# Optimization experiments

Measured on AMD Instinct MI355X. Metric: run time of the kernel, lower is better.

The kernel has to match this reference:

```python
import jax, jax.numpy as jnp
import numpy as np

B, IN, OUT = 128, 1024, 1024
BETA, THRESHOLD, RESET = 0.99, 1.0, 0.8
TAU_POS, TAU_NEG = 20.0, 20.0
A_POS, A_NEG = 0.005, 0.005


def setup_inputs() -> dict:
    key = jax.random.key(0)
    k1, k2, k3, k4, k5 = jax.random.split(key, 5)
    in_spikes = (jax.random.uniform(k1, (B, IN)) < 0.1).astype(jnp.float32)
    # nn.Linear default init: U(-1/sqrt(in), 1/sqrt(in))
    bound = 1.0 / np.sqrt(IN)
    W = jax.random.uniform(k2, (OUT, IN), minval=-bound, maxval=bound, dtype=jnp.float32)
    membrane = jax.random.normal(k3, (B, OUT), dtype=jnp.float32) * 0.5
    # trace timers (time since last spike), random in [0, 50)
    delta_pre = jax.random.uniform(k4, (B, IN), dtype=jnp.float32) * 50.0
    delta_fire = jax.random.uniform(k5, (B, OUT), dtype=jnp.float32) * 50.0
    return {"in_spikes": in_spikes, "W": W, "membrane": membrane,
            "delta_pre": delta_pre, "delta_fire": delta_fire}


def reference(in_spikes, W, membrane, delta_pre, delta_fire):
    # dense projection (bias is unused in the original forward)
    weighted = jnp.matmul(in_spikes, W.T)                      # (B, OUT)
    # LIF neuron
    mem = membrane * BETA + weighted
    spike = (mem > THRESHOLD).astype(jnp.float32)
    mem = jnp.where(spike > 0, mem - RESET, mem)
    # trace updates: increment, reset-to-zero where a spike occurred
    dp = jnp.where(in_spikes > 0, 0.0, delta_pre + 1.0)        # (B, IN)
    df = jnp.where(spike > 0, 0.0, delta_fire + 1.0)           # (B, OUT)
    # pairwise timing difference: (B, IN, OUT)
    delta_t = df[:, None, :] - dp[:, :, None]
    potentiation = (delta_t > 0) * (A_POS * jnp.exp(-delta_t / TAU_POS))
    depression = (delta_t < 0) * (A_NEG * jnp.exp(delta_t / TAU_NEG))
    weight_changes = potentiation - depression                 # (B, IN, OUT)
    avg_weight_changes = weight_changes.mean(axis=0).T         # (OUT, IN)
    new_W = W + avg_weight_changes
    return spike, new_W, mem
```

## Files before the change

kernel.cpp:

```cpp
#include <hip/hip_runtime.h>
#include <cstdint>
#include <cmath>

#define Bb   128
#define INN  1024
#define OUTN 1024
#define A_TOT   (0.005f / 128.0f)
#define INV_TAU (1.0f / 20.0f)

__device__ __forceinline__ uint32_t rne_bf16(float f) {
    uint32_t u = __float_as_uint(f);
    return (u + 0x7fffu + ((u >> 16) & 1u)) >> 16;
}

__global__ __launch_bounds__(256) void prep_k(
    const float* __restrict__ W, const float* __restrict__ in_spikes,
    const float* __restrict__ delta_pre,
    float* __restrict__ Wt, uint32_t* __restrict__ IPackT,
    int* __restrict__ gIdx, int* __restrict__ gCount) {
    __shared__ float tile[32][33];
    const int blk = blockIdx.x;
    const int t   = threadIdx.x;

    if ((blk & 3) == 0 && t < 64) {
        const int b = blk >> 2;
        int base = 0;
#pragma unroll
        for (int c = 0; c < 16; c++) {
            float s = in_spikes[(size_t)b * INN + c * 64 + t];
            unsigned long long m = __ballot(s > 0.0f);
            if (s > 0.0f) {
                int pos = base + __popcll(m & ((1ULL << t) - 1ULL));
                gIdx[b * INN + pos] = c * 64 + t;
            }
            base += __popcll(m);
        }
        if (t == 0) gCount[b] = base;
    }

    {
        const int e = blk * 256 + t;
        const int b = e >> 10, i = e & 1023;
        float sp = in_spikes[e];
        float dp = (sp > 0.0f) ? 0.0f : delta_pre[e] + 1.0f;
        float Iz = expf(-dp * INV_TAU);
        float Iy = A_TOT * expf(dp * INV_TAU);
        IPackT[(size_t)i * Bb + b] = (rne_bf16(Iz) << 16) | rne_bf16(Iy);
    }

    const int x = t & 31, y = t >> 5;
#pragma unroll
    for (int k = 0; k < 2; k++) {
        int tau = blk * 2 + k;
        int bx = tau & 31, by = tau >> 5;
        __syncthreads();
#pragma unroll
        for (int j = 0; j < 4; j++)
            tile[y + j * 8][x] = W[(size_t)(by * 32 + y + j * 8) * INN + bx * 32 + x];
        __syncthreads();
#pragma unroll
        for (int j = 0; j < 4; j++)
            Wt[(size_t)(bx * 32 + y + j * 8) * OUTN + by * 32 + x] = tile[x][y + j * 8];
    }
}

__global__ __launch_bounds__(256) void spmv_lif_k(
    const float* __restrict__ Wt, const float* __restrict__ membrane,
    const float* __restrict__ delta_fire,
    const int* __restrict__ gIdx, const int* __restrict__ gCount,
    uint32_t* __restrict__ OPackT,
    float* __restrict__ out_spike, float* __restrict__ out_mem) {
    __shared__ int sIdx[INN];
    const int b = blockIdx.x;
    const int z = blockIdx.y;
    const int t = threadIdx.x;
    const int n = gCount[b];
    for (int j = t; j < n; j += 256) sIdx[j] = gIdx[b * INN + j];
    __syncthreads();

    const int o = z * 256 + t;
    float acc = 0.0f;
    int j = 0;
    for (; j + 8 <= n; j += 8) {
        float w0 = Wt[(size_t)sIdx[j + 0] * OUTN + o];
        float w1 = Wt[(size_t)sIdx[j + 1] * OUTN + o];
        float w2 = Wt[(size_t)sIdx[j + 2] * OUTN + o];
        float w3 = Wt[(size_t)sIdx[j + 3] * OUTN + o];
        float w4 = Wt[(size_t)sIdx[j + 4] * OUTN + o];
        float w5 = Wt[(size_t)sIdx[j + 5] * OUTN + o];
        float w6 = Wt[(size_t)sIdx[j + 6] * OUTN + o];
        float w7 = Wt[(size_t)sIdx[j + 7] * OUTN + o];
        acc += ((w0 + w1) + (w2 + w3)) + ((w4 + w5) + (w6 + w7));
    }
    for (; j < n; j++) acc += Wt[(size_t)sIdx[j] * OUTN + o];

    const int n_bo = b * OUTN + o;
    float mem = membrane[n_bo] * 0.99f + acc;
    float s = (mem > 1.0f) ? 1.0f : 0.0f;
    mem = (s > 0.0f) ? mem - 0.8f : mem;
    out_spike[n_bo] = s;
    out_mem[n_bo] = mem;

    float df = (s > 0.0f) ? 0.0f : delta_fire[n_bo] + 1.0f;
    float Oy = expf(-df * INV_TAU);
    float Oz = -A_TOT * expf(df * INV_TAU);
    OPackT[(size_t)o * Bb + b] = (rne_bf16(Oy) << 16) | rne_bf16(Oz);
}

__global__ __launch_bounds__(256, 4) void stdp_k(
    const float* __restrict__ W, const uint32_t* __restrict__ OPackT,
    const uint32_t* __restrict__ IPackT, float* __restrict__ outW) {
    __shared__ uint32_t sOT[32 * 32];
    __shared__ uint32_t sIT[32 * 32];
    const int t  = threadIdx.x;
    const int o0 = blockIdx.x * 32;
    const int i0 = blockIdx.y * 32;
    const int tx = t & 15;
    const int ty = t >> 4;
    const int srow = t >> 3;
    const int sc   = t & 7;
    const int swr  = (srow >> 1) & 7;
    const int so = ty & 7, si = tx & 7;

    float acc[2][2] = {{0.f, 0.f}, {0.f, 0.f}};

    for (int cb = 0; cb < Bb / 32; cb++) {
        const int b0 = cb * 32;
        *(uint4*)&sOT[srow * 32 + ((sc ^ swr) << 2)] =
            *(const uint4*)&OPackT[(size_t)(o0 + srow) * Bb + b0 + 4 * sc];
        *(uint4*)&sIT[srow * 32 + ((sc ^ swr) << 2)] =
            *(const uint4*)&IPackT[(size_t)(i0 + srow) * Bb + b0 + 4 * sc];
        __syncthreads();

#pragma unroll
        for (int c4 = 0; c4 < 8; c4++) {
            const int co = (c4 ^ so) << 2;
            const int ci = (c4 ^ si) << 2;
            uint4 oA = *(const uint4*)&sOT[(2 * ty + 0) * 32 + co];
            uint4 oB = *(const uint4*)&sOT[(2 * ty + 1) * 32 + co];
            uint4 iA = *(const uint4*)&sIT[(2 * tx + 0) * 32 + ci];
            uint4 iB = *(const uint4*)&sIT[(2 * tx + 1) * 32 + ci];
            const uint32_t ovA[4] = {oA.x, oA.y, oA.z, oA.w};
            const uint32_t ovB[4] = {oB.x, oB.y, oB.z, oB.w};
            const uint32_t ivA[4] = {iA.x, iA.y, iA.z, iA.w};
            const uint32_t ivB[4] = {iB.x, iB.y, iB.z, iB.w};
#pragma unroll
            for (int k = 0; k < 4; k++) {
                uint32_t k00 = min(ovA[k], ivA[k]);
                uint32_t p00 = max(ovA[k], ivA[k]) << 16;
                acc[0][0] = fmaf(__uint_as_float(k00), __uint_as_float(p00),
                                 acc[0][0]);
                uint32_t k01 = min(ovA[k], ivB[k]);
                uint32_t p01 = max(ovA[k], ivB[k]) << 16;
                acc[0][1] = fmaf(__uint_as_float(k01), __uint_as_float(p01),
                                 acc[0][1]);
                uint32_t k10 = min(ovB[k], ivA[k]);
                uint32_t p10 = max(ovB[k], ivA[k]) << 16;
                acc[1][0] = fmaf(__uint_as_float(k10), __uint_as_float(p10),
                                 acc[1][0]);
                uint32_t k11 = min(ovB[k], ivB[k]);
                uint32_t p11 = max(ovB[k], ivB[k]) << 16;
                acc[1][1] = fmaf(__uint_as_float(k11), __uint_as_float(p11),
                                 acc[1][1]);
            }
        }
        __syncthreads();
    }

#pragma unroll
    for (int a = 0; a < 2; a++) {
        const size_t off = (size_t)(o0 + 2 * ty + a) * INN + i0 + 2 * tx;
        float2 w = *(const float2*)&W[off];
        *(float2*)&outW[off] = make_float2(w.x + acc[a][0], w.y + acc[a][1]);
    }
}

extern "C" void kernel_launch(void* const* d_in, const int* in_sizes, int n_in,
                              void* d_out, int out_size, void* d_ws, size_t ws_size,
                              hipStream_t stream) {
    const float* in_spikes  = (const float*)d_in[0];
    const float* W          = (const float*)d_in[1];
    const float* membrane   = (const float*)d_in[2];
    const float* delta_pre  = (const float*)d_in[3];
    const float* delta_fire = (const float*)d_in[4];

    float* out_spike = (float*)d_out;
    float* out_W     = out_spike + (size_t)Bb * OUTN;
    float* out_mem   = out_W + (size_t)OUTN * INN;

    float* ws        = (float*)d_ws;
    float* Wt        = ws;
    uint32_t* OPackT = (uint32_t*)(Wt + (size_t)INN * OUTN);
    uint32_t* IPackT = OPackT + (size_t)OUTN * Bb;
    int* gIdx        = (int*)(IPackT + (size_t)INN * Bb);
    int* gCount      = gIdx + (size_t)Bb * INN;

    hipLaunchKernelGGL(prep_k, dim3(512), dim3(256), 0, stream,
                       W, in_spikes, delta_pre, Wt, IPackT, gIdx, gCount);
    hipLaunchKernelGGL(spmv_lif_k, dim3(Bb, 4), dim3(256), 0, stream,
                       Wt, membrane, delta_fire, gIdx, gCount,
                       OPackT, out_spike, out_mem);
    hipLaunchKernelGGL(stdp_k, dim3(OUTN / 32, INN / 32), dim3(256), 0, stream,
                       W, OPackT, IPackT, out_W);
}
```

Baseline: 99.93 us.

## Retile STDP kernel to 64x64 blocks with 8x8 register tiles and split-K reduction

Rewrites the STDP outer-product kernel so each block covers a 64x64 (out,in) tile with the full batch staged once in shared memory. Each wavefront handles a quarter of the batch and each thread computes an 8x8 register tile, and the four partial sums are combined through shared memory in the epilogue. This raises arithmetic intensity per LDS load and cuts the grid from 1024 blocks to 256, removing per-chunk barriers. The cost is much higher register pressure (64 accumulators plus 16 uint4 operands), 64KB of LDS per block, and only one block per CU, so occupancy drops.

```diff
diff --git a/kernel.cpp b/kernel.cpp
--- a/kernel.cpp
+++ b/kernel.cpp
@@ -107,71 +107,83 @@
     OPackT[(size_t)o * Bb + b] = (rne_bf16(Oy) << 16) | rne_bf16(Oz);
 }
 
-__global__ __launch_bounds__(256, 4) void stdp_k(
+__global__ __launch_bounds__(256, 1) void stdp_k(
     const float* __restrict__ W, const uint32_t* __restrict__ OPackT,
     const uint32_t* __restrict__ IPackT, float* __restrict__ outW) {
-    __shared__ uint32_t sOT[32 * 32];
-    __shared__ uint32_t sIT[32 * 32];
-    const int t  = threadIdx.x;
-    const int o0 = blockIdx.x * 32;
-    const int i0 = blockIdx.y * 32;
-    const int tx = t & 15;
-    const int ty = t >> 4;
-    const int srow = t >> 3;
-    const int sc   = t & 7;
-    const int swr  = (srow >> 1) & 7;
-    const int so = ty & 7, si = tx & 7;
-
-    float acc[2][2] = {{0.f, 0.f}, {0.f, 0.f}};
-
-    for (int cb = 0; cb < Bb / 32; cb++) {
-        const int b0 = cb * 32;
-        *(uint4*)&sOT[srow * 32 + ((sc ^ swr) << 2)] =
-            *(const uint4*)&OPackT[(size_t)(o0 + srow) * Bb + b0 + 4 * sc];
-        *(uint4*)&sIT[srow * 32 + ((sc ^ swr) << 2)] =
-            *(const uint4*)&IPackT[(size_t)(i0 + srow) * Bb + b0 + 4 * sc];
-        __syncthreads();
-
-#pragma unroll
-        for (int c4 = 0; c4 < 8; c4++) {
-            const int co = (c4 ^ so) << 2;
-            const int ci = (c4 ^ si) << 2;
-            uint4 oA = *(const uint4*)&sOT[(2 * ty + 0) * 32 + co];
-            uint4 oB = *(const uint4*)&sOT[(2 * ty + 1) * 32 + co];
-            uint4 iA = *(const uint4*)&sIT[(2 * tx + 0) * 32 + ci];
-            uint4 iB = *(const uint4*)&sIT[(2 * tx + 1) * 32 + ci];
-            const uint32_t ovA[4] = {oA.x, oA.y, oA.z, oA.w};
-            const uint32_t ovB[4] = {oB.x, oB.y, oB.z, oB.w};
-            const uint32_t ivA[4] = {iA.x, iA.y, iA.z, iA.w};
-            const uint32_t ivB[4] = {iB.x, iB.y, iB.z, iB.w};
-#pragma unroll
-            for (int k = 0; k < 4; k++) {
-                uint32_t k00 = min(ovA[k], ivA[k]);
-                uint32_t p00 = max(ovA[k], ivA[k]) << 16;
-                acc[0][0] = fmaf(__uint_as_float(k00), __uint_as_float(p00),
-                                 acc[0][0]);
-                uint32_t k01 = min(ovA[k], ivB[k]);
-                uint32_t p01 = max(ovA[k], ivB[k]) << 16;
-                acc[0][1] = fmaf(__uint_as_float(k01), __uint_as_float(p01),
-                                 acc[0][1]);
-                uint32_t k10 = min(ovB[k], ivA[k]);
-                uint32_t p10 = max(ovB[k], ivA[k]) << 16;
-                acc[1][0] = fmaf(__uint_as_float(k10), __uint_as_float(p10),
-                                 acc[1][0]);
-                uint32_t k11 = min(ovB[k], ivB[k]);
-                uint32_t p11 = max(ovB[k], ivB[k]) << 16;
-                acc[1][1] = fmaf(__uint_as_float(k11), __uint_as_float(p11),
-                                 acc[1][1]);
+    __shared__ uint32_t sm[16384];
+    uint32_t* sOT = sm;
+    uint32_t* sIT = sm + 8192;
+    const int t    = threadIdx.x;
+    const int lane = t & 63, q = t >> 6;
+    const int ly = lane >> 3, lx = lane & 7;
+    const int o0 = (blockIdx.x & 15) * 64;
+    const int i0 = (blockIdx.x >> 4) * 64;
+
+#pragma unroll
+    for (int r = 0; r < 8; r++) {
+        const int idx = r * 256 + t;
+        const int row = idx >> 5, c = idx & 31;
+        const int cs = (c ^ (row >> 3)) << 2;
+        *(uint4*)&sOT[row * 128 + cs] =
+            *(const uint4*)&OPackT[(size_t)(o0 + row) * Bb + c * 4];
+        *(uint4*)&sIT[row * 128 + cs] =
+            *(const uint4*)&IPackT[(size_t)(i0 + row) * Bb + c * 4];
+    }
+    __syncthreads();
+
+    float acc[8][8];
+#pragma unroll
+    for (int a = 0; a < 8; a++)
+#pragma unroll
+        for (int c = 0; c < 8; c++) acc[a][c] = 0.0f;
+
+#pragma unroll 2
+    for (int s = 0; s < 8; s++) {
+        const int cq = q * 8 + s;
+        uint4 ov[8], iv[8];
+#pragma unroll
+        for (int a = 0; a < 8; a++)
+            ov[a] = *(const uint4*)&sOT[(8 * ly + a) * 128 + ((cq ^ ly) << 2)];
+#pragma unroll
+        for (int c = 0; c < 8; c++)
+            iv[c] = *(const uint4*)&sIT[(8 * lx + c) * 128 + ((cq ^ lx) << 2)];
+#pragma unroll
+        for (int a = 0; a < 8; a++) {
+            const uint32_t oo[4] = {ov[a].x, ov[a].y, ov[a].z, ov[a].w};
+#pragma unroll
+            for (int c = 0; c < 8; c++) {
+                const uint32_t ii[4] = {iv[c].x, iv[c].y, iv[c].z, iv[c].w};
+#pragma unroll
+                for (int k = 0; k < 4; k++) {
+                    uint32_t kk = min(oo[k], ii[k]);
+                    uint32_t pp = max(oo[k], ii[k]) << 16;
+                    acc[a][c] = fmaf(__uint_as_float(kk),
+                                     __uint_as_float(pp), acc[a][c]);
+                }
             }
         }
-        __syncthreads();
-    }
-
-#pragma unroll
-    for (int a = 0; a < 2; a++) {
-        const size_t off = (size_t)(o0 + 2 * ty + a) * INN + i0 + 2 * tx;
-        float2 w = *(const float2*)&W[off];
-        *(float2*)&outW[off] = make_float2(w.x + acc[a][0], w.y + acc[a][1]);
+    }
+    __syncthreads();
+
+    float* epi = (float*)sm;
+#pragma unroll
+    for (int a = 0; a < 8; a++) {
+        const int base = q * 4096 + (8 * ly + a) * 64 + 8 * lx;
+        *(float4*)&epi[base]     = make_float4(acc[a][0], acc[a][1],
+                                               acc[a][2], acc[a][3]);
+        *(float4*)&epi[base + 4] = make_float4(acc[a][4], acc[a][5],
+                                               acc[a][6], acc[a][7]);
+    }
+    __syncthreads();
+
+#pragma unroll
+    for (int j = 0; j < 16; j++) {
+        const int flat = j * 256 + t;
+        const int ol = flat >> 6, il = flat & 63;
+        float v = (epi[flat] + epi[flat + 4096]) +
+                  (epi[flat + 8192] + epi[flat + 12288]);
+        const size_t off = (size_t)(o0 + ol) * INN + i0 + il;
+        outW[off] = W[off] + v;
     }
 }
 
@@ -200,6 +212,6 @@
     hipLaunchKernelGGL(spmv_lif_k, dim3(Bb, 4), dim3(256), 0, stream,
                        Wt, membrane, delta_fire, gIdx, gCount,
                        OPackT, out_spike, out_mem);
-    hipLaunchKernelGGL(stdp_k, dim3(OUTN / 32, INN / 32), dim3(256), 0, stream,
+    hipLaunchKernelGGL(stdp_k, dim3(256), dim3(256), 0, stream,
                        W, OPackT, IPackT, out_W);
 }
```

After: 101.4 us. About the same (+1.4%).
